# Optimization experiments

Measured on AMD Instinct MI355X. Metric: run time of the kernel, lower is better.

The kernel has to match this reference:

```python
import jax, jax.numpy as jnp
import numpy as np

B, T, D, H = 4, 2048, 1024, 8
d = D // H
EPS = 1e-12  # torch F.normalize eps


def _l2norm(x):
    n = jnp.sqrt(jnp.sum(x * x, axis=-1, keepdims=True))
    return x / jnp.maximum(n, EPS)


def setup_inputs() -> dict:
    key = jax.random.key(0)
    ks = jax.random.split(key, 7)
    s = 1.0 / np.sqrt(D)
    return {
        "x": jax.random.normal(ks[0], (B, T, D), dtype=jnp.float32),
        "Wq": jax.random.uniform(ks[1], (D, D), jnp.float32, -s, s),
        "Wk": jax.random.uniform(ks[2], (D, D), jnp.float32, -s, s),
        "Wv": jax.random.uniform(ks[3], (D, D), jnp.float32, -s, s),
        "Wo": jax.random.uniform(ks[4], (D, D), jnp.float32, -s, s),
        "Wlr": jax.random.uniform(ks[5], (D, D), jnp.float32, -s, s),
        "b_lr": jnp.zeros((D,), jnp.float32),
    }


def reference(x, Wq, Wk, Wv, Wo, Wlr, b_lr):
    # projections (torch Linear: y = x @ W.T)
    q = (x @ Wq.T).reshape(B, T, H, d)
    k = _l2norm((x @ Wk.T).reshape(B, T, H, d))
    v = _l2norm((x @ Wv.T).reshape(B, T, H, d))
    lr = jax.nn.sigmoid(x @ Wlr.T + b_lr).reshape(B, T, H, d)

    # scan over time; state w: [B,H,d,d]
    def step(w, qkvl):
        q_t, k_t, v_t, lr_t = qkvl  # each [B,H,d]
        v_old = jnp.einsum('bhij,bhj->bhi', w, k_t)          # retrieve
        w = w + (lr_t * (v_t - v_old))[..., :, None] * k_t[..., None, :]
        o_t = jnp.einsum('bhij,bhj->bhi', w, q_t)            # read
        return w, o_t

    to_t = lambda a: jnp.moveaxis(a, 1, 0)  # [B,T,H,d] -> [T,B,H,d]
    w0 = jnp.zeros((B, H, d, d), dtype=q.dtype)
    _, o = jax.lax.scan(step, w0, (to_t(q), to_t(k), to_t(v), to_t(lr)))
    o = jnp.moveaxis(o, 0, 1).reshape(B, T, D)
    return o @ Wo.T
```

## Files before the change

kernel.cpp:

```cpp
#include <hip/hip_runtime.h>
#include <math.h>

#define Bsz  4
#define Tlen 2048
#define Dm   1024
#define Hh   8
#define dh   128
#define Mrows (Bsz * Tlen)
#define CH   128
#define NCH  (Tlen / CH)
#define C64  64
#define NC64 (Tlen / C64)

typedef __attribute__((ext_vector_type(8))) short  s16x8;
typedef __attribute__((ext_vector_type(4))) float  f32x4;
typedef __attribute__((ext_vector_type(2))) float  f32x2;

__device__ inline unsigned short f2b_rne(float f) {
    unsigned int u = __float_as_uint(f);
    u += 0x7FFFu + ((u >> 16) & 1u);
    return (unsigned short)(u >> 16);
}
__device__ inline float b2f(unsigned short u) {
    return __uint_as_float(((unsigned int)u) << 16);
}

__global__ __launch_bounds__(256) void cvt_f32_bf16(const float* __restrict__ in,
                                                    unsigned short* __restrict__ out)
{
    const size_t i = ((size_t)blockIdx.x * 256 + threadIdx.x) * 4;
    float4 v = *(const float4*)&in[i];
    ushort4 o;
    o.x = f2b_rne(v.x); o.y = f2b_rne(v.y);
    o.z = f2b_rne(v.z); o.w = f2b_rne(v.w);
    *(ushort4*)&out[i] = o;
}

__global__ __launch_bounds__(256) void gemm_bf16(const unsigned short* __restrict__ A,
                                                 const unsigned short* __restrict__ Wt,
                                                 const float* __restrict__ bias,
                                                 float* __restrict__ Yf,
                                                 unsigned short* __restrict__ Y16,
                                                 int mode)
{
    __shared__ __align__(16) unsigned short As[128 * 32];
    __shared__ __align__(16) unsigned short Bs[128 * 32];

    const int tid   = threadIdx.x;
    const int w     = tid >> 6;
    const int lane  = tid & 63;
    const int r4    = lane >> 2;
    const int p4    = lane & 3;
    const int row16 = lane & 15;
    const int quad  = lane >> 4;

    const int m0 = blockIdx.y * 128;
    const int n0 = blockIdx.x * 128;
    const int wm = (w >> 1) * 64;
    const int wn = (w & 1) * 64;

    f32x4 acc[4][4];
#pragma unroll
    for (int i = 0; i < 4; ++i)
#pragma unroll
        for (int j = 0; j < 4; ++j)
            acc[i][j] = (f32x4){0.f, 0.f, 0.f, 0.f};

    for (int k0 = 0; k0 < 1024; k0 += 32) {
        __syncthreads();
#pragma unroll
        for (int c = 0; c < 2; ++c) {
            const int ml  = w * 32 + c * 16 + r4;
            const int swz = (ml >> 1) & 3;
            const unsigned short* ga = A  + (size_t)(m0 + ml) * 1024 + k0 + ((p4 ^ swz) << 3);
            const unsigned short* gb = Wt + (size_t)(n0 + ml) * 1024 + k0 + ((p4 ^ swz) << 3);
            __builtin_amdgcn_global_load_lds(
                (const __attribute__((address_space(1))) void*)ga,
                (__attribute__((address_space(3))) void*)&As[(w * 32 + c * 16) * 32], 16, 0, 0);
            __builtin_amdgcn_global_load_lds(
                (const __attribute__((address_space(1))) void*)gb,
                (__attribute__((address_space(3))) void*)&Bs[(w * 32 + c * 16) * 32], 16, 0, 0);
        }
        __syncthreads();

        s16x8 af[4], bf[4];
#pragma unroll
        for (int bm = 0; bm < 4; ++bm) {
            const int ml  = wm + bm * 16 + row16;
            const int pos = quad ^ ((ml >> 1) & 3);
            af[bm] = *(const s16x8*)&As[ml * 32 + pos * 8];
        }
#pragma unroll
        for (int bn = 0; bn < 4; ++bn) {
            const int nl  = wn + bn * 16 + row16;
            const int pos = quad ^ ((nl >> 1) & 3);
            bf[bn] = *(const s16x8*)&Bs[nl * 32 + pos * 8];
        }
#pragma unroll
        for (int bm = 0; bm < 4; ++bm)
#pragma unroll
            for (int bn = 0; bn < 4; ++bn)
                acc[bm][bn] = __builtin_amdgcn_mfma_f32_16x16x32_bf16(af[bm], bf[bn], acc[bm][bn], 0, 0, 0);
    }

#pragma unroll
    for (int bm = 0; bm < 4; ++bm) {
        const int row = m0 + wm + bm * 16 + quad * 4;
#pragma unroll
        for (int bn = 0; bn < 4; ++bn) {
            const int col = n0 + wn + bn * 16 + row16;
            const float bb = bias ? bias[col] : 0.f;
#pragma unroll
            for (int r = 0; r < 4; ++r) {
                float val = acc[bm][bn][r] + bb;
                if (mode == 1) val = 1.f / (1.f + __expf(-val));
                if (mode == 2) Y16[(size_t)(row + r) * 1024 + col] = f2b_rne(val);
                else           Yf [(size_t)(row + r) * 1024 + col] = val;
            }
        }
    }
}

__global__ __launch_bounds__(256) void l2norm_rows(float* __restrict__ Kb,
                                                   float* __restrict__ Vb,
                                                   unsigned short* __restrict__ K16,
                                                   unsigned short* __restrict__ K16lo)
{
    const int gtid = blockIdx.x * 256 + threadIdx.x;
    const int row  = gtid >> 6;
    const int lane = threadIdx.x & 63;
    const size_t base = (size_t)row * dh + lane * 2;

    float2 k2 = *(float2*)&Kb[base];
    float2 v2 = *(float2*)&Vb[base];
    float sk = k2.x * k2.x + k2.y * k2.y;
    float sv = v2.x * v2.x + v2.y * v2.y;
#pragma unroll
    for (int off = 1; off < 64; off <<= 1) {
        sk += __shfl_xor(sk, off);
        sv += __shfl_xor(sv, off);
    }
    const float rk = 1.f / fmaxf(sqrtf(sk), 1e-12f);
    const float rv = 1.f / fmaxf(sqrtf(sv), 1e-12f);
    k2.x *= rk; k2.y *= rk;
    v2.x *= rv; v2.y *= rv;
    *(float2*)&Kb[base] = k2;
    *(float2*)&Vb[base] = v2;
    const unsigned short hx = f2b_rne(k2.x), hy = f2b_rne(k2.y);
    ((unsigned int*)K16)[base >> 1] = (unsigned int)hx | ((unsigned int)hy << 16);
    const unsigned short lx = f2b_rne(k2.x - b2f(hx));
    const unsigned short ly = f2b_rne(k2.y - b2f(hy));
    ((unsigned int*)K16lo)[base >> 1] = (unsigned int)lx | ((unsigned int)ly << 16);
}

__global__ __launch_bounds__(256) void gram_kt(const unsigned short* __restrict__ K16,
                                               const unsigned short* __restrict__ K16lo,
                                               float* __restrict__ Gf,
                                               unsigned short* __restrict__ KThi,
                                               unsigned short* __restrict__ KTlo)
{
    __shared__ __align__(16) unsigned short Kp[2][64 * 136];

    const int blk = blockIdx.x;
    const int c   = blk & 31;
    const int bh  = blk >> 5;
    const int b   = bh >> 3, h = bh & 7;
    const int tid = threadIdx.x;

    {
        const int row = tid >> 2, seg = (tid & 3) * 32;
        const size_t gsrc = ((size_t)(b * Tlen + c * C64 + row)) * Dm + h * dh + seg;
        const s16x8* ph = (const s16x8*)&K16[gsrc];
        const s16x8* pl = (const s16x8*)&K16lo[gsrc];
#pragma unroll
        for (int q = 0; q < 4; ++q) {
            *(s16x8*)&Kp[0][row * 136 + seg + q * 8] = ph[q];
            *(s16x8*)&Kp[1][row * 136 + seg + q * 8] = pl[q];
        }
    }
    __syncthreads();

    const int w     = tid >> 6;
    const int lane  = tid & 63;
    const int row16 = lane & 15;
    const int quad  = lane >> 4;
    const int sh = (w >> 1) * 32;
    const int th = (w & 1) * 32;

    f32x4 ag[2][2];
#pragma unroll
    for (int i = 0; i < 2; ++i)
#pragma unroll
        for (int j = 0; j < 2; ++j)
            ag[2 > i ? i : i][j] = (f32x4){0.f, 0.f, 0.f, 0.f};

#pragma unroll
    for (int pass = 0; pass < 3; ++pass) {
        const int pa = (pass == 2) ? 1 : 0;
        const int pb = (pass == 1) ? 1 : 0;
#pragma unroll
        for (int k0 = 0; k0 < 128; k0 += 32) {
            s16x8 af[2], bf[2];
#pragma unroll
            for (int bm = 0; bm < 2; ++bm) {
                const int ml = sh + bm * 16 + row16;
                af[bm] = *(const s16x8*)&Kp[pa][ml * 136 + k0 + quad * 8];
            }
#pragma unroll
            for (int bn = 0; bn < 2; ++bn) {
                const int nl = th + bn * 16 + row16;
                bf[bn] = *(const s16x8*)&Kp[pb][nl * 136 + k0 + quad * 8];
            }
#pragma unroll
            for (int bm = 0; bm < 2; ++bm)
#pragma unroll
                for (int bn = 0; bn < 2; ++bn)
                    ag[bm][bn] = __builtin_amdgcn_mfma_f32_16x16x32_bf16(af[bm], bf[bn], ag[bm][bn], 0, 0, 0);
        }
    }

    float* gout = Gf + ((size_t)(bh * 32 + c)) * 4096;
#pragma unroll
    for (int bm = 0; bm < 2; ++bm)
#pragma unroll
        for (int bn = 0; bn < 2; ++bn) {
            const int t = th + bn * 16 + row16;
#pragma unroll
            for (int r = 0; r < 4; ++r) {
                const int s = sh + bm * 16 + quad * 4 + r;
                gout[s * 64 + t] = ag[bm][bn][r];
            }
        }

    {
        const int j   = tid >> 1;
        const int th2 = (tid & 1) * 32;
        unsigned int pk[16];
#pragma unroll
        for (int hl = 0; hl < 2; ++hl) {
#pragma unroll
            for (int p = 0; p < 16; ++p) {
                const unsigned short e0 = Kp[hl][(th2 + 2 * p) * 136 + j];
                const unsigned short e1 = Kp[hl][(th2 + 2 * p + 1) * 136 + j];
                pk[p] = (unsigned int)e0 | ((unsigned int)e1 << 16);
            }
            unsigned short* dst = (hl ? KTlo : KThi) +
                ((size_t)(bh * 32 + c) * 128 + j) * 64 + th2;
#pragma unroll
            for (int q = 0; q < 4; ++q)
                *(uint4*)&dst[q * 8] = *(uint4*)&pk[q * 4];
        }
    }
}

__global__ __launch_bounds__(256) void solve_coef(const unsigned short* __restrict__ K16,
                                                  const float* __restrict__ Vb,
                                                  const float* __restrict__ LRb,
                                                  const float* __restrict__ Gf,
                                                  const unsigned short* __restrict__ KThi,
                                                  const unsigned short* __restrict__ KTlo,
                                                  unsigned short* __restrict__ Ut,
                                                  unsigned short* __restrict__ Wcp)
{
    extern __shared__ __align__(16) char smem[];
    unsigned short* Khs = (unsigned short*)smem;
    unsigned short* Ws  = (unsigned short*)(smem + 16384);
    float*          Gs  = (float*)(smem + 49152);
    unsigned short* Uhi = (unsigned short*)(smem + 65536);
    unsigned short* Ulo = (unsigned short*)(smem + 81920);

    const int bh = blockIdx.x;
    const int b  = bh >> 3, h = bh & 7;
    const int tid   = threadIdx.x;
    const int w     = tid >> 6;
    const int lane  = tid & 63;
    const int p4    = lane & 3;
    const int row16 = lane & 15;
    const int quad  = lane >> 4;
    const int wm = (w >> 1) * 64;
    const int wn = (w & 1) * 64;
    const int ih  = (w >> 1) * 64;
    const int th2 = (w & 1) * 32;

    f32x4 Wa[4][4];
#pragma unroll
    for (int i = 0; i < 4; ++i)
#pragma unroll
        for (int j = 0; j < 4; ++j)
            Wa[i][j] = (f32x4){0.f, 0.f, 0.f, 0.f};

    const int ilane = w * 64 + lane;

#pragma unroll 1
    for (int c = 0; c < NC64; ++c) {
        const int t0g = c * C64;

#pragma unroll
        for (int c4 = 0; c4 < 4; ++c4) {
            const int rr = c4 * 16 + (lane >> 2);
            const unsigned short* ga = K16 + ((size_t)(b * Tlen + t0g + rr)) * Dm + h * dh
                                       + w * 32 + ((p4 ^ ((rr >> 1) & 3)) << 3);
            __builtin_amdgcn_global_load_lds(
                (const __attribute__((address_space(1))) void*)ga,
                (__attribute__((address_space(3))) void*)((char*)Khs + w * 4096 + c4 * 1024 + lane * 16),
                16, 0, 0);
        }
        {
            const size_t gbase = (size_t)(bh * 32 + c) * 4096;
#pragma unroll
            for (int c4 = 0; c4 < 4; ++c4) {
                const float* gg = Gf + gbase + w * 1024 + c4 * 256 + lane * 4;
                __builtin_amdgcn_global_load_lds(
                    (const __attribute__((address_space(1))) void*)gg,
                    (__attribute__((address_space(3))) void*)((char*)Gs + (w * 1024 + c4 * 256 + lane * 4) * 4),
                    16, 0, 0);
            }
        }
#pragma unroll
        for (int bm = 0; bm < 4; ++bm)
#pragma unroll
            for (int bn = 0; bn < 4; ++bn) {
                const int j  = wn + bn * 16 + row16;
                const int sl = j >> 5, jj = j & 31;
#pragma unroll
                for (int r = 0; r < 4; ++r) {
                    const int i = wm + bm * 16 + quad * 4 + r;
                    Ws[sl * 4096 + i * 32 + (((jj >> 3) ^ ((i >> 1) & 3)) << 3) + (j & 7)] =
                        f2b_rne(Wa[bm][bn][r]);
                }
            }
        __syncthreads();

        f32x4 aA[4][2];
#pragma unroll
        for (int i = 0; i < 4; ++i)
#pragma unroll
            for (int j = 0; j < 2; ++j)
                aA[i][j] = (f32x4){0.f, 0.f, 0.f, 0.f};
#pragma unroll
        for (int k0s = 0; k0s < 4; ++k0s) {
            s16x8 af[4], bf[2];
#pragma unroll
            for (int bm = 0; bm < 4; ++bm) {
                const int ml = ih + bm * 16 + row16;
                af[bm] = *(const s16x8*)&Ws[k0s * 4096 + ml * 32 + ((quad ^ ((ml >> 1) & 3)) << 3)];
            }
#pragma unroll
            for (int bn = 0; bn < 2; ++bn) {
                const int nl = th2 + bn * 16 + row16;
                bf[bn] = *(const s16x8*)&Khs[k0s * 2048 + nl * 32 + ((quad ^ ((nl >> 1) & 3)) << 3)];
            }
#pragma unroll
            for (int bm = 0; bm < 4; ++bm)
#pragma unroll
                for (int bn = 0; bn < 2; ++bn)
                    aA[bm][bn] = __builtin_amdgcn_mfma_f32_16x16x32_bf16(af[bm], bf[bn], aA[bm][bn], 0, 0, 0);
        }
        if ((c & 1) == 0) {
            const int i2 = tid >> 1, half = tid & 1;
            unsigned short* dstrow = Wcp + ((size_t)(bh * NCH + (c >> 1)) * 128 + i2) * 128;
#pragma unroll
            for (int sl = 0; sl < 4; ++sl)
#pragma unroll
                for (int gq = 0; gq < 2; ++gq) {
                    const int gg = half * 2 + gq;
                    s16x8 v = *(const s16x8*)&Ws[sl * 4096 + i2 * 32 + ((gg ^ ((i2 >> 1) & 3)) << 3)];
                    *(s16x8*)&dstrow[sl * 32 + gg * 8] = v;
                }
        }
        __syncthreads();

#pragma unroll
        for (int bm = 0; bm < 4; ++bm)
#pragma unroll
            for (int bn = 0; bn < 2; ++bn) {
                const int t = th2 + bn * 16 + row16;
#pragma unroll
                for (int r = 0; r < 4; ++r) {
                    const int i = ih + bm * 16 + quad * 4 + r;
                    Khs[t * 128 + (((i >> 3) ^ (t & 7)) << 3) + (i & 7)] = f2b_rne(aA[bm][bn][r]);
                }
            }
        __syncthreads();

        if (w >= 2) {
            const int base2 = (w - 2) * 2;
#pragma unroll
            for (int bb = 0; bb < 2; ++bb) {
                const int buf = base2 + bb;
                const int st  = buf & 1;
                const unsigned short* src = (buf < 2) ? KThi : KTlo;
#pragma unroll
                for (int c8 = 0; c8 < 8; ++c8) {
                    const int jj = c8 * 16 + (lane >> 2);
                    const unsigned short* ga = src + ((size_t)(bh * 32 + c) * 128 + jj) * 64
                                               + st * 32 + ((p4 ^ ((jj >> 1) & 3)) << 3);
                    __builtin_amdgcn_global_load_lds(
                        (const __attribute__((address_space(1))) void*)ga,
                        (__attribute__((address_space(3))) void*)((char*)Ws + buf * 8192 + c8 * 1024 + lane * 16),
                        16, 0, 0);
                }
            }
        } else {
            const int i = ilane;
            const float* vp  = Vb  + ((size_t)(b * Tlen + t0g)) * Dm + h * dh + i;
            const float* lrp = LRb + ((size_t)(b * Tlen + t0g)) * Dm + h * dh + i;
            f32x4 r4[16];
#pragma unroll
            for (int q = 0; q < 16; ++q) {
#pragma unroll
                for (int e = 0; e < 4; ++e) {
                    const int t = 4 * q + e;
                    const float a0 = b2f(Khs[t * 128 + (((i >> 3) ^ (t & 7)) << 3) + (i & 7)]);
                    r4[q][e] = vp[(size_t)t * Dm] - a0;
                }
            }
            float lv[8], o8[8];
#pragma unroll
            for (int g = 0; g < 8; ++g) {
#pragma unroll
                for (int u = 0; u < 8; ++u)
                    lv[u] = lrp[(size_t)(g * 8 + u) * Dm];
#pragma unroll
                for (int su = 0; su < 8; ++su) {
                    const int s = g * 8 + su;
                    const float cf = lv[su] * r4[s >> 2][s & 3];
                    o8[su] = cf;
                    const f32x4 cf4 = (f32x4){cf, cf, cf, cf};
#pragma unroll
                    for (int q = 2 * g; q < 16; ++q) {
                        const f32x4 g4 = *(const f32x4*)&Gs[s * 64 + q * 4];
                        r4[q] -= cf4 * g4;
                    }
                }
                unsigned int phi[4], plo[4];
#pragma unroll
                for (int qq = 0; qq < 4; ++qq) {
                    const unsigned short h0 = f2b_rne(o8[2 * qq]);
                    const unsigned short h1 = f2b_rne(o8[2 * qq + 1]);
                    const unsigned short l0 = f2b_rne(o8[2 * qq] - b2f(h0));
                    const unsigned short l1 = f2b_rne(o8[2 * qq + 1] - b2f(h1));
                    phi[qq] = (unsigned int)h0 | ((unsigned int)h1 << 16);
                    plo[qq] = (unsigned int)l0 | ((unsigned int)l1 << 16);
                }
                const int lg = g ^ (i & 7);
                *(uint4*)&Uhi[i * 64 + (lg << 3)] = *(uint4*)phi;
                *(uint4*)&Ulo[i * 64 + (lg << 3)] = *(uint4*)plo;
                *(uint4*)&Ut[(size_t)(bh * 128 + i) * Tlen + t0g + 8 * g] = *(uint4*)phi;
            }
        }
        __syncthreads();

#pragma unroll
        for (int pass = 0; pass < 3; ++pass) {
            const unsigned short* Ua = (pass == 1) ? Ulo : Uhi;
            const int bufbase = (pass == 2) ? 2 : 0;
#pragma unroll
            for (int st = 0; st < 2; ++st) {
                s16x8 af[4], bf[4];
#pragma unroll
                for (int bm = 0; bm < 4; ++bm) {
                    const int ml = wm + bm * 16 + row16;
                    af[bm] = *(const s16x8*)&Ua[ml * 64 + (((st * 4 + quad) ^ (ml & 7)) << 3)];
                }
#pragma unroll
                for (int bn = 0; bn < 4; ++bn) {
                    const int nl = wn + bn * 16 + row16;
                    bf[bn] = *(const s16x8*)&Ws[(bufbase + st) * 4096 + nl * 32 + ((quad ^ ((nl >> 1) & 3)) << 3)];
                }
#pragma unroll
                for (int bm = 0; bm < 4; ++bm)
#pragma unroll
                    for (int bn = 0; bn < 4; ++bn)
                        Wa[bm][bn] = __builtin_amdgcn_mfma_f32_16x16x32_bf16(af[bm], bf[bn], Wa[bm][bn], 0, 0, 0);
            }
        }
        __syncthreads();
    }
}

__global__ __launch_bounds__(256) void chunk_o(const unsigned short* __restrict__ Q16,
                                               const unsigned short* __restrict__ K16,
                                               const unsigned short* __restrict__ Ut,
                                               const unsigned short* __restrict__ Wcp,
                                               unsigned short* __restrict__ Obb)
{
    __shared__ __align__(16) unsigned short As[128 * 32];
    __shared__ __align__(16) unsigned short Bs[128 * 32];
    __shared__ __align__(16) unsigned short Sb[128 * 136];

    const int blk = blockIdx.x;
    const int c   = blk & (NCH - 1);
    const int bh  = blk >> 4;
    const int b   = bh >> 3, h = bh & 7;

    const int tid   = threadIdx.x;
    const int w     = tid >> 6;
    const int lane  = tid & 63;
    const int r4    = lane >> 2;
    const int p4    = lane & 3;
    const int row16 = lane & 15;
    const int quad  = lane >> 4;
    const int wm = (w >> 1) * 64;
    const int wn = (w & 1) * 64;

    const size_t qkbase = (size_t)b * Tlen * Dm + (size_t)(c * CH) * Dm + (size_t)h * dh;
    const size_t ubase  = (size_t)bh * dh * Tlen + (size_t)c * CH;
    const size_t wbase  = ((size_t)bh * NCH + c) * dh * dh;

    f32x4 acc[4][4];
#pragma unroll
    for (int i = 0; i < 4; ++i)
#pragma unroll
        for (int j = 0; j < 4; ++j)
            acc[i][j] = (f32x4){0.f, 0.f, 0.f, 0.f};

    for (int k0 = 0; k0 < 128; k0 += 32) {
        __syncthreads();
#pragma unroll
        for (int cc = 0; cc < 2; ++cc) {
            const int ml  = w * 32 + cc * 16 + r4;
            const int swz = (ml >> 1) & 3;
            const unsigned short* ga = Q16 + qkbase + (size_t)ml * Dm + k0 + ((p4 ^ swz) << 3);
            const unsigned short* gb = K16 + qkbase + (size_t)ml * Dm + k0 + ((p4 ^ swz) << 3);
            __builtin_amdgcn_global_load_lds(
                (const __attribute__((address_space(1))) void*)ga,
                (__attribute__((address_space(3))) void*)&As[(w * 32 + cc * 16) * 32], 16, 0, 0);
            __builtin_amdgcn_global_load_lds(
                (const __attribute__((address_space(1))) void*)gb,
                (__attribute__((address_space(3))) void*)&Bs[(w * 32 + cc * 16) * 32], 16, 0, 0);
        }
        __syncthreads();

        s16x8 af[4], bf[4];
#pragma unroll
        for (int bm = 0; bm < 4; ++bm) {
            const int ml  = wm + bm * 16 + row16;
            const int pos = quad ^ ((ml >> 1) & 3);
            af[bm] = *(const s16x8*)&As[ml * 32 + pos * 8];
        }
#pragma unroll
        for (int bn = 0; bn < 4; ++bn) {
            const int nl  = wn + bn * 16 + row16;
            const int pos = quad ^ ((nl >> 1) & 3);
            bf[bn] = *(const s16x8*)&Bs[nl * 32 + pos * 8];
        }
#pragma unroll
        for (int bm = 0; bm < 4; ++bm)
#pragma unroll
            for (int bn = 0; bn < 4; ++bn)
                acc[bm][bn] = __builtin_amdgcn_mfma_f32_16x16x32_bf16(af[bm], bf[bn], acc[bm][bn], 0, 0, 0);
    }

#pragma unroll
    for (int bm = 0; bm < 4; ++bm) {
#pragma unroll
        for (int bn = 0; bn < 4; ++bn) {
            const int s_loc = wn + bn * 16 + row16;
#pragma unroll
            for (int r = 0; r < 4; ++r) {
                const int t_loc = wm + bm * 16 + quad * 4 + r;
                const float val = (s_loc <= t_loc) ? acc[bm][bn][r] : 0.f;
                Sb[t_loc * 136 + s_loc] = f2b_rne(val);
            }
            acc[bm][bn] = (f32x4){0.f, 0.f, 0.f, 0.f};
        }
    }

    for (int k0 = 0; k0 < 128; k0 += 32) {
        __syncthreads();
#pragma unroll
        for (int cc = 0; cc < 2; ++cc) {
            const int nl  = w * 32 + cc * 16 + r4;
            const int swz = (nl >> 1) & 3;
            const unsigned short* gb = Ut + ubase + (size_t)nl * Tlen + k0 + ((p4 ^ swz) << 3);
            __builtin_amdgcn_global_load_lds(
                (const __attribute__((address_space(1))) void*)gb,
                (__attribute__((address_space(3))) void*)&Bs[(w * 32 + cc * 16) * 32], 16, 0, 0);
        }
        __syncthreads();

        s16x8 af[4], bf[4];
#pragma unroll
        for (int bm = 0; bm < 4; ++bm) {
            const int ml = wm + bm * 16 + row16;
            af[bm] = *(const s16x8*)&Sb[ml * 136 + k0 + quad * 8];
        }
#pragma unroll
        for (int bn = 0; bn < 4; ++bn) {
            const int nl  = wn + bn * 16 + row16;
            const int pos = quad ^ ((nl >> 1) & 3);
            bf[bn] = *(const s16x8*)&Bs[nl * 32 + pos * 8];
        }
#pragma unroll
        for (int bm = 0; bm < 4; ++bm)
#pragma unroll
            for (int bn = 0; bn < 4; ++bn)
                acc[bm][bn] = __builtin_amdgcn_mfma_f32_16x16x32_bf16(af[bm], bf[bn], acc[bm][bn], 0, 0, 0);
    }

    for (int k0 = 0; k0 < 128; k0 += 32) {
        __syncthreads();
#pragma unroll
        for (int cc = 0; cc < 2; ++cc) {
            const int ml  = w * 32 + cc * 16 + r4;
            const int swz = (ml >> 1) & 3;
            const unsigned short* ga = Q16 + qkbase + (size_t)ml * Dm + k0 + ((p4 ^ swz) << 3);
            const unsigned short* gb = Wcp + wbase + (size_t)ml * dh + k0 + ((p4 ^ swz) << 3);
            __builtin_amdgcn_global_load_lds(
                (const __attribute__((address_space(1))) void*)ga,
                (__attribute__((address_space(3))) void*)&As[(w * 32 + cc * 16) * 32], 16, 0, 0);
            __builtin_amdgcn_global_load_lds(
                (const __attribute__((address_space(1))) void*)gb,
                (__attribute__((address_space(3))) void*)&Bs[(w * 32 + cc * 16) * 32], 16, 0, 0);
        }
        __syncthreads();

        s16x8 af[4], bf[4];
#pragma unroll
        for (int bm = 0; bm < 4; ++bm) {
            const int ml  = wm + bm * 16 + row16;
            const int pos = quad ^ ((ml >> 1) & 3);
            af[bm] = *(const s16x8*)&As[ml * 32 + pos * 8];
        }
#pragma unroll
        for (int bn = 0; bn < 4; ++bn) {
            const int nl  = wn + bn * 16 + row16;
            const int pos = quad ^ ((nl >> 1) & 3);
            bf[bn] = *(const s16x8*)&Bs[nl * 32 + pos * 8];
        }
#pragma unroll
        for (int bm = 0; bm < 4; ++bm)
#pragma unroll
            for (int bn = 0; bn < 4; ++bn)
                acc[bm][bn] = __builtin_amdgcn_mfma_f32_16x16x32_bf16(af[bm], bf[bn], acc[bm][bn], 0, 0, 0);
    }

#pragma unroll
    for (int bm = 0; bm < 4; ++bm) {
#pragma unroll
        for (int bn = 0; bn < 4; ++bn) {
            const int i_loc = wn + bn * 16 + row16;
#pragma unroll
            for (int r = 0; r < 4; ++r) {
                const int t_loc = wm + bm * 16 + quad * 4 + r;
                Obb[qkbase + (size_t)t_loc * Dm + i_loc] = f2b_rne(acc[bm][bn][r]);
            }
        }
    }
}

extern "C" void kernel_launch(void* const* d_in, const int* in_sizes, int n_in,
                              void* d_out, int out_size, void* d_ws, size_t ws_size,
                              hipStream_t stream)
{
    const float* x    = (const float*)d_in[0];
    const float* Wq   = (const float*)d_in[1];
    const float* Wk   = (const float*)d_in[2];
    const float* Wv   = (const float*)d_in[3];
    const float* Wo   = (const float*)d_in[4];
    const float* Wlr  = (const float*)d_in[5];
    const float* b_lr = (const float*)d_in[6];

    float* ws = (float*)d_ws;
    const size_t S  = (size_t)Mrows * Dm;
    const size_t SW = (size_t)Dm * Dm;
    float* Kb  = ws;
    float* Vb  = ws + S;
    float* LRb = ws + 2 * S;
    unsigned short* xb   = (unsigned short*)(ws + 3 * S);
    unsigned short* Wcp  = xb;
    unsigned short* Q16  = xb + S;
    unsigned short* K16  = Q16 + S;
    unsigned short* Ut   = K16 + S;
    unsigned short* Obb  = Ut + S;
    unsigned short* Wqb  = Obb + S;
    unsigned short* Wkb  = Wqb + SW;
    unsigned short* Wvb  = Wkb + SW;
    unsigned short* Wlrb = Wvb + SW;
    unsigned short* Wob  = Wlrb + SW;
    unsigned short* K16lo = Ut;
    float*          Gf    = (float*)Obb;
    unsigned short* KThi  = (unsigned short*)Kb;
    unsigned short* KTlo  = KThi + S;

    static int attr_done = 0;
    if (!attr_done) {
        (void)hipFuncSetAttribute((const void*)solve_coef,
                                  hipFuncAttributeMaxDynamicSharedMemorySize, 98304);
        attr_done = 1;
    }

    cvt_f32_bf16<<<S / 1024, 256, 0, stream>>>(x, xb);
    cvt_f32_bf16<<<SW / 1024, 256, 0, stream>>>(Wq, Wqb);
    cvt_f32_bf16<<<SW / 1024, 256, 0, stream>>>(Wk, Wkb);
    cvt_f32_bf16<<<SW / 1024, 256, 0, stream>>>(Wv, Wvb);
    cvt_f32_bf16<<<SW / 1024, 256, 0, stream>>>(Wlr, Wlrb);
    cvt_f32_bf16<<<SW / 1024, 256, 0, stream>>>(Wo, Wob);

    dim3 gg(Dm / 128, Mrows / 128);
    gemm_bf16<<<gg, 256, 0, stream>>>(xb, Wqb, nullptr, nullptr, Q16, 2);
    gemm_bf16<<<gg, 256, 0, stream>>>(xb, Wkb, nullptr, Kb, nullptr, 0);
    gemm_bf16<<<gg, 256, 0, stream>>>(xb, Wvb, nullptr, Vb, nullptr, 0);
    gemm_bf16<<<gg, 256, 0, stream>>>(xb, Wlrb, b_lr, LRb, nullptr, 1);

    l2norm_rows<<<(Bsz * Tlen * Hh) / 4, 256, 0, stream>>>(Kb, Vb, K16, K16lo);

    gram_kt<<<32 * 32, 256, 0, stream>>>(K16, K16lo, Gf, KThi, KTlo);

    solve_coef<<<32, 256, 98304, stream>>>(K16, Vb, LRb, Gf, KThi, KTlo, Ut, Wcp);

    chunk_o<<<Bsz * Hh * NCH, 256, 0, stream>>>(Q16, K16, Ut, Wcp, Obb);

    gemm_bf16<<<gg, 256, 0, stream>>>(Obb, Wob, nullptr, (float*)d_out, nullptr, 0);
}
```

Measured before the change: 698.4 us.

## Double-buffer K and Gram loads in solve_coef and widen to 512 threads

The sequential solve_coef kernel, which runs only 32 blocks, now uses 8 waves instead of 4. Each MFMA wave owns half as many W rows. Dedicated waves prefetch the next chunk's K tile and Gram matrix into double-buffered LDS while two waves run the triangular solve, which removes load latency from the serial chunk loop. The Wcp snapshot is now written straight from the accumulator conversion, and the Ut stores are batched after the solve. LDS use grows to 144KB, and the direct Wcp writes are scalar 2-byte global stores.

```diff
diff --git a/kernel.cpp b/kernel.cpp
--- a/kernel.cpp
+++ b/kernel.cpp
@@ -14,7 +14,6 @@
 
 typedef __attribute__((ext_vector_type(8))) short  s16x8;
 typedef __attribute__((ext_vector_type(4))) float  f32x4;
-typedef __attribute__((ext_vector_type(2))) float  f32x2;
 
 __device__ inline unsigned short f2b_rne(float f) {
     unsigned int u = __float_as_uint(f);
@@ -192,7 +191,7 @@
     for (int i = 0; i < 2; ++i)
 #pragma unroll
         for (int j = 0; j < 2; ++j)
-            ag[2 > i ? i : i][j] = (f32x4){0.f, 0.f, 0.f, 0.f};
+            ag[i][j] = (f32x4){0.f, 0.f, 0.f, 0.f};
 
 #pragma unroll
     for (int pass = 0; pass < 3; ++pass) {
@@ -253,7 +252,7 @@
     }
 }
 
-__global__ __launch_bounds__(256) void solve_coef(const unsigned short* __restrict__ K16,
+__global__ __launch_bounds__(512) void solve_coef(const unsigned short* __restrict__ K16,
                                                   const float* __restrict__ Vb,
                                                   const float* __restrict__ LRb,
                                                   const float* __restrict__ Gf,
@@ -263,11 +262,16 @@
                                                   unsigned short* __restrict__ Wcp)
 {
     extern __shared__ __align__(16) char smem[];
-    unsigned short* Khs = (unsigned short*)smem;
-    unsigned short* Ws  = (unsigned short*)(smem + 16384);
-    float*          Gs  = (float*)(smem + 49152);
-    unsigned short* Uhi = (unsigned short*)(smem + 65536);
-    unsigned short* Ulo = (unsigned short*)(smem + 81920);
+    unsigned short* Khs[2];
+    Khs[0] = (unsigned short*)smem;
+    Khs[1] = (unsigned short*)(smem + 16384);
+    unsigned short* Ws  = (unsigned short*)(smem + 32768);
+    float* Gs[2];
+    Gs[0] = (float*)(smem + 65536);
+    Gs[1] = (float*)(smem + 81920);
+    unsigned short* As0 = (unsigned short*)(smem + 98304);
+    unsigned short* Uhi = (unsigned short*)(smem + 114688);
+    unsigned short* Ulo = (unsigned short*)(smem + 131072);
 
     const int bh = blockIdx.x;
     const int b  = bh >> 3, h = bh & 7;
@@ -277,47 +281,55 @@
     const int p4    = lane & 3;
     const int row16 = lane & 15;
     const int quad  = lane >> 4;
-    const int wm = (w >> 1) * 64;
-    const int wn = (w & 1) * 64;
-    const int ih  = (w >> 1) * 64;
+    const int wm  = (w >> 1) * 32;
+    const int wn  = (w & 1) * 64;
     const int th2 = (w & 1) * 32;
 
-    f32x4 Wa[4][4];
-#pragma unroll
-    for (int i = 0; i < 4; ++i)
+    f32x4 Wa[2][4];
+#pragma unroll
+    for (int i = 0; i < 2; ++i)
 #pragma unroll
         for (int j = 0; j < 4; ++j)
             Wa[i][j] = (f32x4){0.f, 0.f, 0.f, 0.f};
 
     const int ilane = w * 64 + lane;
+
+    if (w == 5) {
+#pragma unroll
+        for (int sl = 0; sl < 4; ++sl)
+#pragma unroll
+            for (int c4 = 0; c4 < 4; ++c4) {
+                const int rr = c4 * 16 + (lane >> 2);
+                const unsigned short* ga = K16 + ((size_t)(b * Tlen + rr)) * Dm + h * dh
+                                           + sl * 32 + ((p4 ^ ((rr >> 1) & 3)) << 3);
+                __builtin_amdgcn_global_load_lds(
+                    (const __attribute__((address_space(1))) void*)ga,
+                    (__attribute__((address_space(3))) void*)((char*)Khs[0] + sl * 4096 + c4 * 1024 + lane * 16),
+                    16, 0, 0);
+            }
+    }
+    if (w == 4 || w == 6) {
+        const size_t gbase = (size_t)(bh * 32 + 0) * 4096;
+        const int half = (w == 6) ? 8 : 0;
+#pragma unroll
+        for (int c4 = 0; c4 < 8; ++c4) {
+            const int seg = half + c4;
+            const float* gg = Gf + gbase + seg * 256 + lane * 4;
+            __builtin_amdgcn_global_load_lds(
+                (const __attribute__((address_space(1))) void*)gg,
+                (__attribute__((address_space(3))) void*)((char*)Gs[0] + (seg * 256 + lane * 4) * 4),
+                16, 0, 0);
+        }
+    }
+    __syncthreads();
 
 #pragma unroll 1
     for (int c = 0; c < NC64; ++c) {
         const int t0g = c * C64;
-
-#pragma unroll
-        for (int c4 = 0; c4 < 4; ++c4) {
-            const int rr = c4 * 16 + (lane >> 2);
-            const unsigned short* ga = K16 + ((size_t)(b * Tlen + t0g + rr)) * Dm + h * dh
-                                       + w * 32 + ((p4 ^ ((rr >> 1) & 3)) << 3);
-            __builtin_amdgcn_global_load_lds(
-                (const __attribute__((address_space(1))) void*)ga,
-                (__attribute__((address_space(3))) void*)((char*)Khs + w * 4096 + c4 * 1024 + lane * 16),
-                16, 0, 0);
-        }
-        {
-            const size_t gbase = (size_t)(bh * 32 + c) * 4096;
-#pragma unroll
-            for (int c4 = 0; c4 < 4; ++c4) {
-                const float* gg = Gf + gbase + w * 1024 + c4 * 256 + lane * 4;
-                __builtin_amdgcn_global_load_lds(
-                    (const __attribute__((address_space(1))) void*)gg,
-                    (__attribute__((address_space(3))) void*)((char*)Gs + (w * 1024 + c4 * 256 + lane * 4) * 4),
-                    16, 0, 0);
-            }
-        }
-#pragma unroll
-        for (int bm = 0; bm < 4; ++bm)
+        const int cur = c & 1;
+
+#pragma unroll
+        for (int bm = 0; bm < 2; ++bm)
 #pragma unroll
             for (int bn = 0; bn < 4; ++bn) {
                 const int j  = wn + bn * 16 + row16;
@@ -325,65 +337,55 @@
 #pragma unroll
                 for (int r = 0; r < 4; ++r) {
                     const int i = wm + bm * 16 + quad * 4 + r;
-                    Ws[sl * 4096 + i * 32 + (((jj >> 3) ^ ((i >> 1) & 3)) << 3) + (j & 7)] =
-                        f2b_rne(Wa[bm][bn][r]);
-                }
-            }
-        __syncthreads();
-
-        f32x4 aA[4][2];
-#pragma unroll
-        for (int i = 0; i < 4; ++i)
-#pragma unroll
-            for (int j = 0; j < 2; ++j)
-                aA[i][j] = (f32x4){0.f, 0.f, 0.f, 0.f};
-#pragma unroll
-        for (int k0s = 0; k0s < 4; ++k0s) {
-            s16x8 af[4], bf[2];
-#pragma unroll
-            for (int bm = 0; bm < 4; ++bm) {
-                const int ml = ih + bm * 16 + row16;
-                af[bm] = *(const s16x8*)&Ws[k0s * 4096 + ml * 32 + ((quad ^ ((ml >> 1) & 3)) << 3)];
-            }
-#pragma unroll
-            for (int bn = 0; bn < 2; ++bn) {
-                const int nl = th2 + bn * 16 + row16;
-                bf[bn] = *(const s16x8*)&Khs[k0s * 2048 + nl * 32 + ((quad ^ ((nl >> 1) & 3)) << 3)];
-            }
-#pragma unroll
-            for (int bm = 0; bm < 4; ++bm)
-#pragma unroll
-                for (int bn = 0; bn < 2; ++bn)
-                    aA[bm][bn] = __builtin_amdgcn_mfma_f32_16x16x32_bf16(af[bm], bf[bn], aA[bm][bn], 0, 0, 0);
-        }
-        if ((c & 1) == 0) {
-            const int i2 = tid >> 1, half = tid & 1;
-            unsigned short* dstrow = Wcp + ((size_t)(bh * NCH + (c >> 1)) * 128 + i2) * 128;
-#pragma unroll
-            for (int sl = 0; sl < 4; ++sl)
-#pragma unroll
-                for (int gq = 0; gq < 2; ++gq) {
-                    const int gg = half * 2 + gq;
-                    s16x8 v = *(const s16x8*)&Ws[sl * 4096 + i2 * 32 + ((gg ^ ((i2 >> 1) & 3)) << 3)];
-                    *(s16x8*)&dstrow[sl * 32 + gg * 8] = v;
-                }
-        }
-        __syncthreads();
-
-#pragma unroll
-        for (int bm = 0; bm < 4; ++bm)
-#pragma unroll
-            for (int bn = 0; bn < 2; ++bn) {
-                const int t = th2 + bn * 16 + row16;
-#pragma unroll
-                for (int r = 0; r < 4; ++r) {
-                    const int i = ih + bm * 16 + quad * 4 + r;
-                    Khs[t * 128 + (((i >> 3) ^ (t & 7)) << 3) + (i & 7)] = f2b_rne(aA[bm][bn][r]);
-                }
-            }
-        __syncthreads();
-
-        if (w >= 2) {
+                    const unsigned short hv = f2b_rne(Wa[bm][bn][r]);
+                    Ws[sl * 4096 + i * 32 + (((jj >> 3) ^ ((i >> 1) & 3)) << 3) + (j & 7)] = hv;
+                    if ((c & 1) == 0)
+                        Wcp[((size_t)(bh * NCH + (c >> 1)) * 128 + i) * 128 + j] = hv;
+                }
+            }
+        __syncthreads();
+
+        {
+            f32x4 aA[2][2];
+#pragma unroll
+            for (int i = 0; i < 2; ++i)
+#pragma unroll
+                for (int j = 0; j < 2; ++j)
+                    aA[i][j] = (f32x4){0.f, 0.f, 0.f, 0.f};
+#pragma unroll
+            for (int k0s = 0; k0s < 4; ++k0s) {
+                s16x8 af[2], bf[2];
+#pragma unroll
+                for (int bm = 0; bm < 2; ++bm) {
+                    const int ml = wm + bm * 16 + row16;
+                    af[bm] = *(const s16x8*)&Ws[k0s * 4096 + ml * 32 + ((quad ^ ((ml >> 1) & 3)) << 3)];
+                }
+#pragma unroll
+                for (int bn = 0; bn < 2; ++bn) {
+                    const int nl = th2 + bn * 16 + row16;
+                    bf[bn] = *(const s16x8*)&Khs[cur][k0s * 2048 + nl * 32 + ((quad ^ ((nl >> 1) & 3)) << 3)];
+                }
+#pragma unroll
+                for (int bm = 0; bm < 2; ++bm)
+#pragma unroll
+                    for (int bn = 0; bn < 2; ++bn)
+                        aA[bm][bn] = __builtin_amdgcn_mfma_f32_16x16x32_bf16(af[bm], bf[bn], aA[bm][bn], 0, 0, 0);
+            }
+#pragma unroll
+            for (int bm = 0; bm < 2; ++bm)
+#pragma unroll
+                for (int bn = 0; bn < 2; ++bn) {
+                    const int t = th2 + bn * 16 + row16;
+#pragma unroll
+                    for (int r = 0; r < 4; ++r) {
+                        const int i = wm + bm * 16 + quad * 4 + r;
+                        As0[t * 128 + (((i >> 3) ^ (t & 7)) << 3) + (i & 7)] = f2b_rne(aA[bm][bn][r]);
+                    }
+                }
+        }
+        __syncthreads();
+
+        if (w == 2 || w == 3) {
             const int base2 = (w - 2) * 2;
 #pragma unroll
             for (int bb = 0; bb < 2; ++bb) {
@@ -401,21 +403,52 @@
                         16, 0, 0);
                 }
             }
-        } else {
+        } else if (w == 5) {
+            if (c + 1 < NC64) {
+#pragma unroll
+                for (int sl = 0; sl < 4; ++sl)
+#pragma unroll
+                    for (int c4 = 0; c4 < 4; ++c4) {
+                        const int rr = c4 * 16 + (lane >> 2);
+                        const unsigned short* ga = K16 + ((size_t)(b * Tlen + t0g + C64 + rr)) * Dm + h * dh
+                                                   + sl * 32 + ((p4 ^ ((rr >> 1) & 3)) << 3);
+                        __builtin_amdgcn_global_load_lds(
+                            (const __attribute__((address_space(1))) void*)ga,
+                            (__attribute__((address_space(3))) void*)((char*)Khs[cur ^ 1] + sl * 4096 + c4 * 1024 + lane * 16),
+                            16, 0, 0);
+                    }
+            }
+        } else if (w == 4 || w == 6) {
+            if (c + 1 < NC64) {
+                const size_t gbase = (size_t)(bh * 32 + c + 1) * 4096;
+                const int half = (w == 6) ? 8 : 0;
+#pragma unroll
+                for (int c4 = 0; c4 < 8; ++c4) {
+                    const int seg = half + c4;
+                    const float* gg = Gf + gbase + seg * 256 + lane * 4;
+                    __builtin_amdgcn_global_load_lds(
+                        (const __attribute__((address_space(1))) void*)gg,
+                        (__attribute__((address_space(3))) void*)((char*)Gs[cur ^ 1] + (seg * 256 + lane * 4) * 4),
+                        16, 0, 0);
+                }
+            }
+        } else if (w < 2) {
             const int i = ilane;
             const float* vp  = Vb  + ((size_t)(b * Tlen + t0g)) * Dm + h * dh + i;
             const float* lrp = LRb + ((size_t)(b * Tlen + t0g)) * Dm + h * dh + i;
+            const float* gs  = Gs[cur];
             f32x4 r4[16];
 #pragma unroll
             for (int q = 0; q < 16; ++q) {
 #pragma unroll
                 for (int e = 0; e < 4; ++e) {
                     const int t = 4 * q + e;
-                    const float a0 = b2f(Khs[t * 128 + (((i >> 3) ^ (t & 7)) << 3) + (i & 7)]);
+                    const float a0 = b2f(As0[t * 128 + (((i >> 3) ^ (t & 7)) << 3) + (i & 7)]);
                     r4[q][e] = vp[(size_t)t * Dm] - a0;
                 }
             }
             float lv[8], o8[8];
+            unsigned int allphi[8][4];
 #pragma unroll
             for (int g = 0; g < 8; ++g) {
 #pragma unroll
@@ -429,25 +462,28 @@
                     const f32x4 cf4 = (f32x4){cf, cf, cf, cf};
 #pragma unroll
                     for (int q = 2 * g; q < 16; ++q) {
-                        const f32x4 g4 = *(const f32x4*)&Gs[s * 64 + q * 4];
+                        const f32x4 g4 = *(const f32x4*)&gs[s * 64 + q * 4];
                         r4[q] -= cf4 * g4;
                     }
                 }
-                unsigned int phi[4], plo[4];
+                unsigned int plo[4];
 #pragma unroll
                 for (int qq = 0; qq < 4; ++qq) {
                     const unsigned short h0 = f2b_rne(o8[2 * qq]);
                     const unsigned short h1 = f2b_rne(o8[2 * qq + 1]);
                     const unsigned short l0 = f2b_rne(o8[2 * qq] - b2f(h0));
                     const unsigned short l1 = f2b_rne(o8[2 * qq + 1] - b2f(h1));
-                    phi[qq] = (unsigned int)h0 | ((unsigned int)h1 << 16);
+                    allphi[g][qq] = (unsigned int)h0 | ((unsigned int)h1 << 16);
                     plo[qq] = (unsigned int)l0 | ((unsigned int)l1 << 16);
                 }
                 const int lg = g ^ (i & 7);
-                *(uint4*)&Uhi[i * 64 + (lg << 3)] = *(uint4*)phi;
+                *(uint4*)&Uhi[i * 64 + (lg << 3)] = *(uint4*)allphi[g];
                 *(uint4*)&Ulo[i * 64 + (lg << 3)] = *(uint4*)plo;
-                *(uint4*)&Ut[(size_t)(bh * 128 + i) * Tlen + t0g + 8 * g] = *(uint4*)phi;
-            }
+            }
+            unsigned short* utrow = Ut + (size_t)(bh * 128 + i) * Tlen + t0g;
+#pragma unroll
+            for (int g = 0; g < 8; ++g)
+                *(uint4*)&utrow[8 * g] = *(uint4*)allphi[g];
         }
         __syncthreads();
 
@@ -457,9 +493,9 @@
             const int bufbase = (pass == 2) ? 2 : 0;
 #pragma unroll
             for (int st = 0; st < 2; ++st) {
-                s16x8 af[4], bf[4];
-#pragma unroll
-                for (int bm = 0; bm < 4; ++bm) {
+                s16x8 af[2], bf[4];
+#pragma unroll
+                for (int bm = 0; bm < 2; ++bm) {
                     const int ml = wm + bm * 16 + row16;
                     af[bm] = *(const s16x8*)&Ua[ml * 64 + (((st * 4 + quad) ^ (ml & 7)) << 3)];
                 }
@@ -469,7 +505,7 @@
                     bf[bn] = *(const s16x8*)&Ws[(bufbase + st) * 4096 + nl * 32 + ((quad ^ ((nl >> 1) & 3)) << 3)];
                 }
 #pragma unroll
-                for (int bm = 0; bm < 4; ++bm)
+                for (int bm = 0; bm < 2; ++bm)
 #pragma unroll
                     for (int bn = 0; bn < 4; ++bn)
                         Wa[bm][bn] = __builtin_amdgcn_mfma_f32_16x16x32_bf16(af[bm], bf[bn], Wa[bm][bn], 0, 0, 0);
@@ -687,7 +723,7 @@
     static int attr_done = 0;
     if (!attr_done) {
         (void)hipFuncSetAttribute((const void*)solve_coef,
-                                  hipFuncAttributeMaxDynamicSharedMemorySize, 98304);
+                                  hipFuncAttributeMaxDynamicSharedMemorySize, 147456);
         attr_done = 1;
     }
 
@@ -708,7 +744,7 @@
 
     gram_kt<<<32 * 32, 256, 0, stream>>>(K16, K16lo, Gf, KThi, KTlo);
 
-    solve_coef<<<32, 256, 98304, stream>>>(K16, Vb, LRb, Gf, KThi, KTlo, Ut, Wcp);
+    solve_coef<<<32, 512, 147456, stream>>>(K16, Vb, LRb, Gf, KThi, KTlo, Ut, Wcp);
 
     chunk_o<<<Bsz * Hh * NCH, 256, 0, stream>>>(Q16, K16, Ut, Wcp, Obb);
 
```

Measured after the change: 1.169 ms. 67.4% more time.
